# Performance work log

Measured on AMD Instinct MI355X. Metric: run time of the kernel, lower is better.

The kernel has to match this reference:

```python
import jax, jax.numpy as jnp
import numpy as np

N_NODES = 50000
N_EDGES = 640000
D_IN = 128
D_HID = 128
D_OUT = 128


def setup_inputs() -> dict:
    key = jax.random.key(0)
    k1, k2, k3, k4 = jax.random.split(key, 4)
    x = jax.random.normal(k1, (N_NODES, D_IN), dtype=jnp.float32)
    edge_index = jax.random.randint(k2, (2, N_EDGES), 0, N_NODES, dtype=jnp.int32)
    W1 = jax.random.normal(k3, (D_IN, D_HID), dtype=jnp.float32) * (1.0 / np.sqrt(D_IN))
    b1 = jnp.zeros((D_HID,), dtype=jnp.float32)
    W2 = jax.random.normal(k4, (D_HID, D_OUT), dtype=jnp.float32) * (1.0 / np.sqrt(D_HID))
    b2 = jnp.zeros((D_OUT,), dtype=jnp.float32)
    return {"x": x, "edge_index": edge_index, "W1": W1, "b1": b1, "W2": W2, "b2": b2}


def gcn_conv(x, edge_index, W, b, num_nodes):
    # PyG GCNConv: add self-loops, symmetric normalization, linear, aggregate, bias.
    loops = jnp.arange(num_nodes, dtype=edge_index.dtype)
    src = jnp.concatenate([edge_index[0], loops])  # source j
    dst = jnp.concatenate([edge_index[1], loops])  # target i
    deg = jax.ops.segment_sum(jnp.ones_like(dst, dtype=x.dtype), dst,
                              num_segments=num_nodes)  # in-degree incl. self-loop
    dinv = jnp.where(deg > 0, jax.lax.rsqrt(deg), 0.0)
    norm = dinv[src] * dinv[dst]  # [E+N]
    h = x @ W  # [N, hidden]
    msg = norm[:, None] * h[src]  # gather + scale
    out = jax.ops.segment_sum(msg, dst, num_segments=num_nodes)  # scatter-add
    return out + b


def reference(x, edge_index, W1, b1, W2, b2):
    h = gcn_conv(x, edge_index, W1, b1, x.shape[0])
    h = jnp.tanh(h)
    return h @ W2 + b2
```

## Files before the change

kernel.cpp:

```cpp
#include <hip/hip_runtime.h>


#define DFEAT 128
#define CAP 48
#define BROWS 32

typedef __attribute__((ext_vector_type(8))) short short8;
typedef __attribute__((ext_vector_type(4))) float float4v;

__device__ __forceinline__ float bflo(unsigned int u) {
    union { unsigned int i; float f; } v; v.i = u << 16; return v.f;
}
__device__ __forceinline__ float bfhi(unsigned int u) {
    union { unsigned int i; float f; } v; v.i = u & 0xffff0000u; return v.f;
}
__device__ __forceinline__ unsigned short f2bf(float f) {
    union { unsigned int i; float f; } v; v.f = f;
    unsigned int r = v.i + 0x7fffu + ((v.i >> 16) & 1u);
    return (unsigned short)(r >> 16);
}
__device__ __forceinline__ unsigned int pack2(float a, float b) {
    return (unsigned int)f2bf(a) | ((unsigned int)f2bf(b) << 16);
}
__device__ __forceinline__ float fast_tanh(float x) {
    float e = __expf(2.0f * x);
    float r = __builtin_amdgcn_rcpf(e + 1.0f);
    return __builtin_fmaf(-2.0f, r, 1.0f);
}

__global__ void k_count_scatter(const int* __restrict__ src, const int* __restrict__ dst,
                                int* __restrict__ cnt, int* __restrict__ col,
                                const float* __restrict__ W1, const float* __restrict__ W2,
                                unsigned short* __restrict__ w1f, unsigned short* __restrict__ w2f,
                                int e) {
    int i = blockIdx.x * blockDim.x + threadIdx.x;
    if (i < 2 * DFEAT * DFEAT) {
        int which = i >> 14;
        int idx = i & 16383;
        int k = idx >> 7, nn = idx & 127;
        int f = ((nn >> 4) << 2) + (k >> 5);
        int lane = (nn & 15) | (((k >> 3) & 3) << 4);
        int j = k & 7;
        int o = f * 512 + lane * 8 + j;
        if (which == 0) w1f[o] = f2bf(W1[idx]);
        else            w2f[o] = f2bf(W2[idx]);
    }
    if (i >= e) return;
    int d = dst[i];
    int p = atomicAdd(&cnt[d], 1);
    if (p < CAP) col[d * CAP + p] = src[i];
}

__global__ void k_prep(const float* __restrict__ x, const int* __restrict__ cnt,
                       unsigned int* __restrict__ xb2, int* __restrict__ col, int n) {
    int i = blockIdx.x * blockDim.x + threadIdx.x;
    if (i < n * 32) {
        float di = rsqrtf((float)(cnt[i >> 5] + 1));
        float4 v = ((const float4*)x)[i];
        xb2[i * 2]     = pack2(v.x * di, v.y * di);
        xb2[i * 2 + 1] = pack2(v.z * di, v.w * di);
    } else if (i < (n + 1) * 32) {
        xb2[i * 2] = 0u;
        xb2[i * 2 + 1] = 0u;
    }
    if (i < n) {
        int d = min(cnt[i], CAP);
        int dpad = (d + 3) & ~3;
        for (int p = d; p < dpad; ++p) col[i * CAP + p] = n;
    }
}

__global__ __launch_bounds__(256) void k_agg_gemm(
    const uint4* __restrict__ xb4, const int* __restrict__ cnt,
    const int* __restrict__ col,
    const unsigned short* __restrict__ w1f, const float* __restrict__ b1,
    const unsigned short* __restrict__ w2f, const float* __restrict__ b2,
    float* __restrict__ out, int n) {
    __shared__ unsigned short aggs[BROWS * 136];
    __shared__ unsigned short hs[BROWS * 136];
    const int t = threadIdx.x;

    const int lane16 = t & 15;
    const int sub = t >> 4;
    for (int g = 0; g < BROWS / 16; ++g) {
        int node_local = g * 16 + sub;
        int node = blockIdx.x * BROWS + node_local;
        int nodec = min(node, n - 1);
        uint4 v = xb4[(size_t)nodec * 16 + lane16];
        float a0 = bflo(v.x), a1 = bfhi(v.x), a2 = bflo(v.y), a3 = bfhi(v.y);
        float a4 = bflo(v.z), a5 = bfhi(v.z), a6 = bflo(v.w), a7 = bfhi(v.w);
        int deg = min(cnt[nodec], CAP);
        const int4* col4 = (const int4*)(col + (size_t)nodec * CAP);
        int nq = (deg + 3) >> 2;
        for (int q = 0; q < nq; ++q) {
            int4 s4 = col4[q];
            uint4 u0 = xb4[(size_t)s4.x * 16 + lane16];
            uint4 u1 = xb4[(size_t)s4.y * 16 + lane16];
            uint4 u2 = xb4[(size_t)s4.z * 16 + lane16];
            uint4 u3 = xb4[(size_t)s4.w * 16 + lane16];
            a0 += bflo(u0.x); a1 += bfhi(u0.x); a2 += bflo(u0.y); a3 += bfhi(u0.y);
            a4 += bflo(u0.z); a5 += bfhi(u0.z); a6 += bflo(u0.w); a7 += bfhi(u0.w);
            a0 += bflo(u1.x); a1 += bfhi(u1.x); a2 += bflo(u1.y); a3 += bfhi(u1.y);
            a4 += bflo(u1.z); a5 += bfhi(u1.z); a6 += bflo(u1.w); a7 += bfhi(u1.w);
            a0 += bflo(u2.x); a1 += bfhi(u2.x); a2 += bflo(u2.y); a3 += bfhi(u2.y);
            a4 += bflo(u2.z); a5 += bfhi(u2.z); a6 += bflo(u2.w); a7 += bfhi(u2.w);
            a0 += bflo(u3.x); a1 += bfhi(u3.x); a2 += bflo(u3.y); a3 += bfhi(u3.y);
            a4 += bflo(u3.z); a5 += bfhi(u3.z); a6 += bflo(u3.w); a7 += bfhi(u3.w);
        }
        float di = rsqrtf((float)(deg + 1));
        uint4 o;
        o.x = pack2(a0 * di, a1 * di);
        o.y = pack2(a2 * di, a3 * di);
        o.z = pack2(a4 * di, a5 * di);
        o.w = pack2(a6 * di, a7 * di);
        *(uint4*)&aggs[node_local * 136 + lane16 * 8] = o;
    }
    __syncthreads();

    const int wave = t >> 6, l = t & 63;
    const int strip = wave >> 1;
    const int colh = wave & 1;
    const int kq = l >> 4;
    const int lc = l & 15;
    const int row_local = strip * 16 + lc;

    float4v acc[4];
    for (int ct = 0; ct < 4; ++ct) acc[ct] = (float4v){0.f, 0.f, 0.f, 0.f};
    for (int kc = 0; kc < 4; ++kc) {
        short8 a = *(const short8*)(aggs + row_local * 136 + kc * 32 + kq * 8);
        for (int ct = 0; ct < 4; ++ct) {
            int ctg = colh * 4 + ct;
            short8 b = *(const short8*)(w1f + (ctg * 4 + kc) * 512 + l * 8);
            acc[ct] = __builtin_amdgcn_mfma_f32_16x16x32_bf16(a, b, acc[ct], 0, 0, 0);
        }
    }
    const int drow0 = strip * 16 + kq * 4;
    for (int ct = 0; ct < 4; ++ct) {
        int c = colh * 64 + ct * 16 + lc;
        float bb = b1[c];
        for (int r = 0; r < 4; ++r) {
            float v = fast_tanh(acc[ct][r] + bb);
            hs[(drow0 + r) * 136 + c] = f2bf(v);
        }
    }
    __syncthreads();

    float4v acc2[4];
    for (int ct = 0; ct < 4; ++ct) acc2[ct] = (float4v){0.f, 0.f, 0.f, 0.f};
    for (int kc = 0; kc < 4; ++kc) {
        short8 a = *(const short8*)(hs + row_local * 136 + kc * 32 + kq * 8);
        for (int ct = 0; ct < 4; ++ct) {
            int ctg = colh * 4 + ct;
            short8 b = *(const short8*)(w2f + (ctg * 4 + kc) * 512 + l * 8);
            acc2[ct] = __builtin_amdgcn_mfma_f32_16x16x32_bf16(a, b, acc2[ct], 0, 0, 0);
        }
    }
    const int orow0 = blockIdx.x * BROWS + drow0;
    for (int ct = 0; ct < 4; ++ct) {
        int c = colh * 64 + ct * 16 + lc;
        float bb = b2[c];
        for (int r = 0; r < 4; ++r) {
            int orow = orow0 + r;
            if (orow < n) out[(size_t)orow * DFEAT + c] = acc2[ct][r] + bb;
        }
    }
}

static inline size_t align256(size_t v) { return (v + 255) & ~(size_t)255; }

extern "C" void kernel_launch(void* const* d_in, const int* in_sizes, int n_in,
                              void* d_out, int out_size, void* d_ws, size_t ws_size,
                              hipStream_t stream) {
    const float* x  = (const float*)d_in[0];
    const int*   ei = (const int*)d_in[1];
    const float* W1 = (const float*)d_in[2];
    const float* b1 = (const float*)d_in[3];
    const float* W2 = (const float*)d_in[4];
    const float* b2 = (const float*)d_in[5];
    float* out = (float*)d_out;

    const int N = in_sizes[0] / DFEAT;
    const int E = in_sizes[1] / 2;
    const int* src = ei;
    const int* dst = ei + E;

    char* ws = (char*)d_ws;
    size_t off = 0;
    int* cnt = (int*)(ws + off);  off += align256((size_t)N * 4);
    int* col = (int*)(ws + off);  off += align256((size_t)N * CAP * 4);
    unsigned short* xb  = (unsigned short*)(ws + off); off += align256((size_t)(N + 1) * DFEAT * 2);
    unsigned short* w1f = (unsigned short*)(ws + off); off += align256((size_t)DFEAT * DFEAT * 2);
    unsigned short* w2f = (unsigned short*)(ws + off); off += align256((size_t)DFEAT * DFEAT * 2);

    hipMemsetAsync(cnt, 0, (size_t)N * 4, stream);
    k_count_scatter<<<(E + 255) / 256, 256, 0, stream>>>(
        src, dst, cnt, col, W1, W2, w1f, w2f, E);
    k_prep<<<((N + 1) * 32 + 255) / 256, 256, 0, stream>>>(
        x, cnt, (unsigned int*)xb, col, N);
    k_agg_gemm<<<(N + BROWS - 1) / BROWS, 256, 0, stream>>>(
        (const uint4*)xb, cnt, col, w1f, b1, w2f, b2, out, N);
}
```

Before: 161.7 us.

## Merge prep into scatter kernel and apply source degree scaling during aggregation

Merges the bf16 conversion of x into the edge-scatter kernel, which removes the separate prep launch, the zero pad row and the padding of column lists. The per-source normalisation dinv[src] is now computed inside the gather loop from cnt, using predicated duplicate indices with zero weight for tail slots. The column index load is software-prefetched one iteration ahead. The trade-off is an extra random cnt load per edge in the aggregation loop, in exchange for one fewer kernel launch and no dependency on the finished degree count before conversion.

```diff
diff --git a/kernel.cpp b/kernel.cpp
--- a/kernel.cpp
+++ b/kernel.cpp
@@ -28,11 +28,12 @@
     return __builtin_fmaf(-2.0f, r, 1.0f);
 }
 
-__global__ void k_count_scatter(const int* __restrict__ src, const int* __restrict__ dst,
-                                int* __restrict__ cnt, int* __restrict__ col,
-                                const float* __restrict__ W1, const float* __restrict__ W2,
-                                unsigned short* __restrict__ w1f, unsigned short* __restrict__ w2f,
-                                int e) {
+__global__ void k_scatter_conv(const int* __restrict__ src, const int* __restrict__ dst,
+                               int* __restrict__ cnt, int* __restrict__ col,
+                               const float* __restrict__ x, unsigned int* __restrict__ xb2,
+                               const float* __restrict__ W1, const float* __restrict__ W2,
+                               unsigned short* __restrict__ w1f, unsigned short* __restrict__ w2f,
+                               int e, int n32) {
     int i = blockIdx.x * blockDim.x + threadIdx.x;
     if (i < 2 * DFEAT * DFEAT) {
         int which = i >> 14;
@@ -45,28 +46,15 @@
         if (which == 0) w1f[o] = f2bf(W1[idx]);
         else            w2f[o] = f2bf(W2[idx]);
     }
-    if (i >= e) return;
-    int d = dst[i];
-    int p = atomicAdd(&cnt[d], 1);
-    if (p < CAP) col[d * CAP + p] = src[i];
-}
-
-__global__ void k_prep(const float* __restrict__ x, const int* __restrict__ cnt,
-                       unsigned int* __restrict__ xb2, int* __restrict__ col, int n) {
-    int i = blockIdx.x * blockDim.x + threadIdx.x;
-    if (i < n * 32) {
-        float di = rsqrtf((float)(cnt[i >> 5] + 1));
+    if (i < e) {
+        int d = dst[i];
+        int p = atomicAdd(&cnt[d], 1);
+        if (p < CAP) col[d * CAP + p] = src[i];
+    }
+    if (i < n32) {
         float4 v = ((const float4*)x)[i];
-        xb2[i * 2]     = pack2(v.x * di, v.y * di);
-        xb2[i * 2 + 1] = pack2(v.z * di, v.w * di);
-    } else if (i < (n + 1) * 32) {
-        xb2[i * 2] = 0u;
-        xb2[i * 2 + 1] = 0u;
-    }
-    if (i < n) {
-        int d = min(cnt[i], CAP);
-        int dpad = (d + 3) & ~3;
-        for (int p = d; p < dpad; ++p) col[i * CAP + p] = n;
+        xb2[i * 2]     = pack2(v.x, v.y);
+        xb2[i * 2 + 1] = pack2(v.z, v.w);
     }
 }
 
@@ -86,28 +74,51 @@
         int node_local = g * 16 + sub;
         int node = blockIdx.x * BROWS + node_local;
         int nodec = min(node, n - 1);
+        int raw = cnt[nodec];
+        int deg = min(raw, CAP);
+        float di = rsqrtf((float)(raw + 1));
         uint4 v = xb4[(size_t)nodec * 16 + lane16];
-        float a0 = bflo(v.x), a1 = bfhi(v.x), a2 = bflo(v.y), a3 = bfhi(v.y);
-        float a4 = bflo(v.z), a5 = bfhi(v.z), a6 = bflo(v.w), a7 = bfhi(v.w);
-        int deg = min(cnt[nodec], CAP);
+        float a0 = bflo(v.x) * di, a1 = bfhi(v.x) * di;
+        float a2 = bflo(v.y) * di, a3 = bfhi(v.y) * di;
+        float a4 = bflo(v.z) * di, a5 = bfhi(v.z) * di;
+        float a6 = bflo(v.w) * di, a7 = bfhi(v.w) * di;
         const int4* col4 = (const int4*)(col + (size_t)nodec * CAP);
         int nq = (deg + 3) >> 2;
+        int4 s4 = col4[0];
         for (int q = 0; q < nq; ++q) {
-            int4 s4 = col4[q];
-            uint4 u0 = xb4[(size_t)s4.x * 16 + lane16];
-            uint4 u1 = xb4[(size_t)s4.y * 16 + lane16];
-            uint4 u2 = xb4[(size_t)s4.z * 16 + lane16];
-            uint4 u3 = xb4[(size_t)s4.w * 16 + lane16];
-            a0 += bflo(u0.x); a1 += bfhi(u0.x); a2 += bflo(u0.y); a3 += bfhi(u0.y);
-            a4 += bflo(u0.z); a5 += bfhi(u0.z); a6 += bflo(u0.w); a7 += bfhi(u0.w);
-            a0 += bflo(u1.x); a1 += bfhi(u1.x); a2 += bflo(u1.y); a3 += bfhi(u1.y);
-            a4 += bflo(u1.z); a5 += bfhi(u1.z); a6 += bflo(u1.w); a7 += bfhi(u1.w);
-            a0 += bflo(u2.x); a1 += bfhi(u2.x); a2 += bflo(u2.y); a3 += bfhi(u2.y);
-            a4 += bflo(u2.z); a5 += bfhi(u2.z); a6 += bflo(u2.w); a7 += bfhi(u2.w);
-            a0 += bflo(u3.x); a1 += bfhi(u3.x); a2 += bflo(u3.y); a3 += bfhi(u3.y);
-            a4 += bflo(u3.z); a5 += bfhi(u3.z); a6 += bflo(u3.w); a7 += bfhi(u3.w);
-        }
-        float di = rsqrtf((float)(deg + 1));
+            int4 nx = col4[min(q + 1, nq - 1)];
+            int b4i = q * 4;
+            bool c1 = (b4i + 1) < deg, c2 = (b4i + 2) < deg, c3 = (b4i + 3) < deg;
+            int i0 = s4.x;
+            int i1 = c1 ? s4.y : i0;
+            int i2 = c2 ? s4.z : i0;
+            int i3 = c3 ? s4.w : i0;
+            float d0 = rsqrtf((float)(cnt[i0] + 1));
+            float d1 = c1 ? rsqrtf((float)(cnt[i1] + 1)) : 0.f;
+            float d2 = c2 ? rsqrtf((float)(cnt[i2] + 1)) : 0.f;
+            float d3 = c3 ? rsqrtf((float)(cnt[i3] + 1)) : 0.f;
+            uint4 u0 = xb4[(size_t)i0 * 16 + lane16];
+            uint4 u1 = xb4[(size_t)i1 * 16 + lane16];
+            uint4 u2 = xb4[(size_t)i2 * 16 + lane16];
+            uint4 u3 = xb4[(size_t)i3 * 16 + lane16];
+            a0 = __builtin_fmaf(bflo(u0.x), d0, a0); a1 = __builtin_fmaf(bfhi(u0.x), d0, a1);
+            a2 = __builtin_fmaf(bflo(u0.y), d0, a2); a3 = __builtin_fmaf(bfhi(u0.y), d0, a3);
+            a4 = __builtin_fmaf(bflo(u0.z), d0, a4); a5 = __builtin_fmaf(bfhi(u0.z), d0, a5);
+            a6 = __builtin_fmaf(bflo(u0.w), d0, a6); a7 = __builtin_fmaf(bfhi(u0.w), d0, a7);
+            a0 = __builtin_fmaf(bflo(u1.x), d1, a0); a1 = __builtin_fmaf(bfhi(u1.x), d1, a1);
+            a2 = __builtin_fmaf(bflo(u1.y), d1, a2); a3 = __builtin_fmaf(bfhi(u1.y), d1, a3);
+            a4 = __builtin_fmaf(bflo(u1.z), d1, a4); a5 = __builtin_fmaf(bfhi(u1.z), d1, a5);
+            a6 = __builtin_fmaf(bflo(u1.w), d1, a6); a7 = __builtin_fmaf(bfhi(u1.w), d1, a7);
+            a0 = __builtin_fmaf(bflo(u2.x), d2, a0); a1 = __builtin_fmaf(bfhi(u2.x), d2, a1);
+            a2 = __builtin_fmaf(bflo(u2.y), d2, a2); a3 = __builtin_fmaf(bfhi(u2.y), d2, a3);
+            a4 = __builtin_fmaf(bflo(u2.z), d2, a4); a5 = __builtin_fmaf(bfhi(u2.z), d2, a5);
+            a6 = __builtin_fmaf(bflo(u2.w), d2, a6); a7 = __builtin_fmaf(bfhi(u2.w), d2, a7);
+            a0 = __builtin_fmaf(bflo(u3.x), d3, a0); a1 = __builtin_fmaf(bfhi(u3.x), d3, a1);
+            a2 = __builtin_fmaf(bflo(u3.y), d3, a2); a3 = __builtin_fmaf(bfhi(u3.y), d3, a3);
+            a4 = __builtin_fmaf(bflo(u3.z), d3, a4); a5 = __builtin_fmaf(bfhi(u3.z), d3, a5);
+            a6 = __builtin_fmaf(bflo(u3.w), d3, a6); a7 = __builtin_fmaf(bfhi(u3.w), d3, a7);
+            s4 = nx;
+        }
         uint4 o;
         o.x = pack2(a0 * di, a1 * di);
         o.y = pack2(a2 * di, a3 * di);
@@ -188,15 +199,17 @@
     size_t off = 0;
     int* cnt = (int*)(ws + off);  off += align256((size_t)N * 4);
     int* col = (int*)(ws + off);  off += align256((size_t)N * CAP * 4);
-    unsigned short* xb  = (unsigned short*)(ws + off); off += align256((size_t)(N + 1) * DFEAT * 2);
+    unsigned short* xb  = (unsigned short*)(ws + off); off += align256((size_t)N * DFEAT * 2);
     unsigned short* w1f = (unsigned short*)(ws + off); off += align256((size_t)DFEAT * DFEAT * 2);
     unsigned short* w2f = (unsigned short*)(ws + off); off += align256((size_t)DFEAT * DFEAT * 2);
 
+    const int n32 = N * 32;
+    int total = n32 > E ? n32 : E;
+    if (total < 2 * DFEAT * DFEAT) total = 2 * DFEAT * DFEAT;
+
     hipMemsetAsync(cnt, 0, (size_t)N * 4, stream);
-    k_count_scatter<<<(E + 255) / 256, 256, 0, stream>>>(
-        src, dst, cnt, col, W1, W2, w1f, w2f, E);
-    k_prep<<<((N + 1) * 32 + 255) / 256, 256, 0, stream>>>(
-        x, cnt, (unsigned int*)xb, col, N);
+    k_scatter_conv<<<(total + 255) / 256, 256, 0, stream>>>(
+        src, dst, cnt, col, x, (unsigned int*)xb, W1, W2, w1f, w2f, E, n32);
     k_agg_gemm<<<(N + BROWS - 1) / BROWS, 256, 0, stream>>>(
         (const uint4*)xb, cnt, col, w1f, b1, w2f, b2, out, N);
 }
```

After: 165.1 us. +2.1%, slower.

## Split CSR build into count and scatter passes; unroll neighbor gather by eight

Applied to the files above, without the earlier changes.

The first kernel now pre-fills the whole neighbor table with the sentinel node index, zeroes a second counter array, and counts in-degrees. The second kernel converts x to scaled bf16 while scattering source indices with a separate atomic counter. Because every unused slot already holds the sentinel, the aggregation loop can fetch two int4 index groups and issue eight independent row gathers per iteration, keeping more loads in flight. The normalization now uses the uncapped degree. The cost is an extra pass of atomics over the edges, a full write of the index table, and some wasted gathers of the zero sentinel row when degrees are padded up to a multiple of eight.

```diff
diff --git a/kernel.cpp b/kernel.cpp
--- a/kernel.cpp
+++ b/kernel.cpp
@@ -28,11 +28,11 @@
     return __builtin_fmaf(-2.0f, r, 1.0f);
 }
 
-__global__ void k_count_scatter(const int* __restrict__ src, const int* __restrict__ dst,
-                                int* __restrict__ cnt, int* __restrict__ col,
-                                const float* __restrict__ W1, const float* __restrict__ W2,
-                                unsigned short* __restrict__ w1f, unsigned short* __restrict__ w2f,
-                                int e) {
+__global__ void k1_count_fill(const int* __restrict__ dst, int* __restrict__ cnt,
+                              int* __restrict__ cnt2, int4* __restrict__ col4,
+                              const float* __restrict__ W1, const float* __restrict__ W2,
+                              unsigned short* __restrict__ w1f, unsigned short* __restrict__ w2f,
+                              int e, int n, int ncol4) {
     int i = blockIdx.x * blockDim.x + threadIdx.x;
     if (i < 2 * DFEAT * DFEAT) {
         int which = i >> 14;
@@ -45,28 +45,33 @@
         if (which == 0) w1f[o] = f2bf(W1[idx]);
         else            w2f[o] = f2bf(W2[idx]);
     }
-    if (i >= e) return;
-    int d = dst[i];
-    int p = atomicAdd(&cnt[d], 1);
-    if (p < CAP) col[d * CAP + p] = src[i];
-}
-
-__global__ void k_prep(const float* __restrict__ x, const int* __restrict__ cnt,
-                       unsigned int* __restrict__ xb2, int* __restrict__ col, int n) {
+    if (i < ncol4) {
+        int4 s; s.x = n; s.y = n; s.z = n; s.w = n;
+        col4[i] = s;
+    }
+    if (i < (n + 3) / 4) ((int4*)cnt2)[i] = (int4){0, 0, 0, 0};
+    if (i < e) atomicAdd(&cnt[dst[i]], 1);
+}
+
+__global__ void k2_scatter_xb(const int* __restrict__ src, const int* __restrict__ dst,
+                              const int* __restrict__ cnt, int* __restrict__ cnt2,
+                              int* __restrict__ col,
+                              const float* __restrict__ x, unsigned int* __restrict__ xb2,
+                              int e, int n32) {
     int i = blockIdx.x * blockDim.x + threadIdx.x;
-    if (i < n * 32) {
+    if (i < n32) {
         float di = rsqrtf((float)(cnt[i >> 5] + 1));
         float4 v = ((const float4*)x)[i];
         xb2[i * 2]     = pack2(v.x * di, v.y * di);
         xb2[i * 2 + 1] = pack2(v.z * di, v.w * di);
-    } else if (i < (n + 1) * 32) {
+    } else if (i < n32 + 32) {
         xb2[i * 2] = 0u;
         xb2[i * 2 + 1] = 0u;
     }
-    if (i < n) {
-        int d = min(cnt[i], CAP);
-        int dpad = (d + 3) & ~3;
-        for (int p = d; p < dpad; ++p) col[i * CAP + p] = n;
+    if (i < e) {
+        int d = dst[i];
+        int p = atomicAdd(&cnt2[d], 1);
+        if (p < CAP) col[d * CAP + p] = src[i];
     }
 }
 
@@ -86,18 +91,25 @@
         int node_local = g * 16 + sub;
         int node = blockIdx.x * BROWS + node_local;
         int nodec = min(node, n - 1);
+        int raw = cnt[nodec];
+        int deg = min(raw, CAP);
+        float di = rsqrtf((float)(raw + 1));
         uint4 v = xb4[(size_t)nodec * 16 + lane16];
         float a0 = bflo(v.x), a1 = bfhi(v.x), a2 = bflo(v.y), a3 = bfhi(v.y);
         float a4 = bflo(v.z), a5 = bfhi(v.z), a6 = bflo(v.w), a7 = bfhi(v.w);
-        int deg = min(cnt[nodec], CAP);
         const int4* col4 = (const int4*)(col + (size_t)nodec * CAP);
-        int nq = (deg + 3) >> 2;
-        for (int q = 0; q < nq; ++q) {
-            int4 s4 = col4[q];
-            uint4 u0 = xb4[(size_t)s4.x * 16 + lane16];
-            uint4 u1 = xb4[(size_t)s4.y * 16 + lane16];
-            uint4 u2 = xb4[(size_t)s4.z * 16 + lane16];
-            uint4 u3 = xb4[(size_t)s4.w * 16 + lane16];
+        int nq2 = (deg + 7) >> 3;
+        for (int q = 0; q < nq2; ++q) {
+            int4 sa = col4[2 * q];
+            int4 sb = col4[2 * q + 1];
+            uint4 u0 = xb4[(size_t)sa.x * 16 + lane16];
+            uint4 u1 = xb4[(size_t)sa.y * 16 + lane16];
+            uint4 u2 = xb4[(size_t)sa.z * 16 + lane16];
+            uint4 u3 = xb4[(size_t)sa.w * 16 + lane16];
+            uint4 u4 = xb4[(size_t)sb.x * 16 + lane16];
+            uint4 u5 = xb4[(size_t)sb.y * 16 + lane16];
+            uint4 u6 = xb4[(size_t)sb.z * 16 + lane16];
+            uint4 u7 = xb4[(size_t)sb.w * 16 + lane16];
             a0 += bflo(u0.x); a1 += bfhi(u0.x); a2 += bflo(u0.y); a3 += bfhi(u0.y);
             a4 += bflo(u0.z); a5 += bfhi(u0.z); a6 += bflo(u0.w); a7 += bfhi(u0.w);
             a0 += bflo(u1.x); a1 += bfhi(u1.x); a2 += bflo(u1.y); a3 += bfhi(u1.y);
@@ -106,8 +118,15 @@
             a4 += bflo(u2.z); a5 += bfhi(u2.z); a6 += bflo(u2.w); a7 += bfhi(u2.w);
             a0 += bflo(u3.x); a1 += bfhi(u3.x); a2 += bflo(u3.y); a3 += bfhi(u3.y);
             a4 += bflo(u3.z); a5 += bfhi(u3.z); a6 += bflo(u3.w); a7 += bfhi(u3.w);
-        }
-        float di = rsqrtf((float)(deg + 1));
+            a0 += bflo(u4.x); a1 += bfhi(u4.x); a2 += bflo(u4.y); a3 += bfhi(u4.y);
+            a4 += bflo(u4.z); a5 += bfhi(u4.z); a6 += bflo(u4.w); a7 += bfhi(u4.w);
+            a0 += bflo(u5.x); a1 += bfhi(u5.x); a2 += bflo(u5.y); a3 += bfhi(u5.y);
+            a4 += bflo(u5.z); a5 += bfhi(u5.z); a6 += bflo(u5.w); a7 += bfhi(u5.w);
+            a0 += bflo(u6.x); a1 += bfhi(u6.x); a2 += bflo(u6.y); a3 += bfhi(u6.y);
+            a4 += bflo(u6.z); a5 += bfhi(u6.z); a6 += bflo(u6.w); a7 += bfhi(u6.w);
+            a0 += bflo(u7.x); a1 += bfhi(u7.x); a2 += bflo(u7.y); a3 += bfhi(u7.y);
+            a4 += bflo(u7.z); a5 += bfhi(u7.z); a6 += bflo(u7.w); a7 += bfhi(u7.w);
+        }
         uint4 o;
         o.x = pack2(a0 * di, a1 * di);
         o.y = pack2(a2 * di, a3 * di);
@@ -186,17 +205,25 @@
 
     char* ws = (char*)d_ws;
     size_t off = 0;
-    int* cnt = (int*)(ws + off);  off += align256((size_t)N * 4);
-    int* col = (int*)(ws + off);  off += align256((size_t)N * CAP * 4);
+    int* cnt  = (int*)(ws + off); off += align256((size_t)N * 4);
+    int* cnt2 = (int*)(ws + off); off += align256((size_t)N * 4);
+    int* col  = (int*)(ws + off); off += align256((size_t)N * CAP * 4);
     unsigned short* xb  = (unsigned short*)(ws + off); off += align256((size_t)(N + 1) * DFEAT * 2);
     unsigned short* w1f = (unsigned short*)(ws + off); off += align256((size_t)DFEAT * DFEAT * 2);
     unsigned short* w2f = (unsigned short*)(ws + off); off += align256((size_t)DFEAT * DFEAT * 2);
 
+    const int ncol4 = N * CAP / 4;
+    const int n32 = N * 32;
+
+    int t1 = E > ncol4 ? E : ncol4;
+    if (t1 < 2 * DFEAT * DFEAT) t1 = 2 * DFEAT * DFEAT;
+    int t2 = (n32 + 32) > E ? (n32 + 32) : E;
+
     hipMemsetAsync(cnt, 0, (size_t)N * 4, stream);
-    k_count_scatter<<<(E + 255) / 256, 256, 0, stream>>>(
-        src, dst, cnt, col, W1, W2, w1f, w2f, E);
-    k_prep<<<((N + 1) * 32 + 255) / 256, 256, 0, stream>>>(
-        x, cnt, (unsigned int*)xb, col, N);
+    k1_count_fill<<<(t1 + 255) / 256, 256, 0, stream>>>(
+        dst, cnt, cnt2, (int4*)col, W1, W2, w1f, w2f, E, N, ncol4);
+    k2_scatter_xb<<<(t2 + 255) / 256, 256, 0, stream>>>(
+        src, dst, cnt, cnt2, col, x, (unsigned int*)xb, E, n32);
     k_agg_gemm<<<(N + BROWS - 1) / BROWS, 256, 0, stream>>>(
         (const uint4*)xb, cnt, col, w1f, b1, w2f, b2, out, N);
 }
```

After: 195.0 us. +20.6%, slower.

## Pad degree counters to separate cache lines and gather eight neighbors per iteration

Applied to the files above, without the earlier changes.

Each node's atomic degree counter is moved to a 64-byte stride so that concurrent atomics on neighbouring nodes no longer contend on the same cache line. The aggregation loop now issues eight neighbour row loads per iteration instead of four, for more memory-level parallelism, and the column lists are padded to multiples of eight with the zero row. The counter buffer and its memset grow sixteenfold, and padding to eight adds wasted gathers for low-degree nodes. The launch size of the first kernel is also made to always cover the weight conversion.

```diff
diff --git a/kernel.cpp b/kernel.cpp
--- a/kernel.cpp
+++ b/kernel.cpp
@@ -3,6 +3,7 @@
 
 #define DFEAT 128
 #define CAP 48
+#define CSTR 16
 #define BROWS 32
 
 typedef __attribute__((ext_vector_type(8))) short short8;
@@ -47,7 +48,7 @@
     }
     if (i >= e) return;
     int d = dst[i];
-    int p = atomicAdd(&cnt[d], 1);
+    int p = atomicAdd(&cnt[d * CSTR], 1);
     if (p < CAP) col[d * CAP + p] = src[i];
 }
 
@@ -55,7 +56,7 @@
                        unsigned int* __restrict__ xb2, int* __restrict__ col, int n) {
     int i = blockIdx.x * blockDim.x + threadIdx.x;
     if (i < n * 32) {
-        float di = rsqrtf((float)(cnt[i >> 5] + 1));
+        float di = rsqrtf((float)(cnt[(i >> 5) * CSTR] + 1));
         float4 v = ((const float4*)x)[i];
         xb2[i * 2]     = pack2(v.x * di, v.y * di);
         xb2[i * 2 + 1] = pack2(v.z * di, v.w * di);
@@ -64,8 +65,8 @@
         xb2[i * 2 + 1] = 0u;
     }
     if (i < n) {
-        int d = min(cnt[i], CAP);
-        int dpad = (d + 3) & ~3;
+        int d = min(cnt[i * CSTR], CAP);
+        int dpad = (d + 7) & ~7;
         for (int p = d; p < dpad; ++p) col[i * CAP + p] = n;
     }
 }
@@ -86,18 +87,25 @@
         int node_local = g * 16 + sub;
         int node = blockIdx.x * BROWS + node_local;
         int nodec = min(node, n - 1);
+        int raw = cnt[nodec * CSTR];
+        int deg = min(raw, CAP);
+        float di = rsqrtf((float)(raw + 1));
         uint4 v = xb4[(size_t)nodec * 16 + lane16];
         float a0 = bflo(v.x), a1 = bfhi(v.x), a2 = bflo(v.y), a3 = bfhi(v.y);
         float a4 = bflo(v.z), a5 = bfhi(v.z), a6 = bflo(v.w), a7 = bfhi(v.w);
-        int deg = min(cnt[nodec], CAP);
         const int4* col4 = (const int4*)(col + (size_t)nodec * CAP);
-        int nq = (deg + 3) >> 2;
-        for (int q = 0; q < nq; ++q) {
-            int4 s4 = col4[q];
-            uint4 u0 = xb4[(size_t)s4.x * 16 + lane16];
-            uint4 u1 = xb4[(size_t)s4.y * 16 + lane16];
-            uint4 u2 = xb4[(size_t)s4.z * 16 + lane16];
-            uint4 u3 = xb4[(size_t)s4.w * 16 + lane16];
+        int nq2 = (deg + 7) >> 3;
+        for (int q = 0; q < nq2; ++q) {
+            int4 sa = col4[2 * q];
+            int4 sb = col4[2 * q + 1];
+            uint4 u0 = xb4[(size_t)sa.x * 16 + lane16];
+            uint4 u1 = xb4[(size_t)sa.y * 16 + lane16];
+            uint4 u2 = xb4[(size_t)sa.z * 16 + lane16];
+            uint4 u3 = xb4[(size_t)sa.w * 16 + lane16];
+            uint4 u4 = xb4[(size_t)sb.x * 16 + lane16];
+            uint4 u5 = xb4[(size_t)sb.y * 16 + lane16];
+            uint4 u6 = xb4[(size_t)sb.z * 16 + lane16];
+            uint4 u7 = xb4[(size_t)sb.w * 16 + lane16];
             a0 += bflo(u0.x); a1 += bfhi(u0.x); a2 += bflo(u0.y); a3 += bfhi(u0.y);
             a4 += bflo(u0.z); a5 += bfhi(u0.z); a6 += bflo(u0.w); a7 += bfhi(u0.w);
             a0 += bflo(u1.x); a1 += bfhi(u1.x); a2 += bflo(u1.y); a3 += bfhi(u1.y);
@@ -106,8 +114,15 @@
             a4 += bflo(u2.z); a5 += bfhi(u2.z); a6 += bflo(u2.w); a7 += bfhi(u2.w);
             a0 += bflo(u3.x); a1 += bfhi(u3.x); a2 += bflo(u3.y); a3 += bfhi(u3.y);
             a4 += bflo(u3.z); a5 += bfhi(u3.z); a6 += bflo(u3.w); a7 += bfhi(u3.w);
-        }
-        float di = rsqrtf((float)(deg + 1));
+            a0 += bflo(u4.x); a1 += bfhi(u4.x); a2 += bflo(u4.y); a3 += bfhi(u4.y);
+            a4 += bflo(u4.z); a5 += bfhi(u4.z); a6 += bflo(u4.w); a7 += bfhi(u4.w);
+            a0 += bflo(u5.x); a1 += bfhi(u5.x); a2 += bflo(u5.y); a3 += bfhi(u5.y);
+            a4 += bflo(u5.z); a5 += bfhi(u5.z); a6 += bflo(u5.w); a7 += bfhi(u5.w);
+            a0 += bflo(u6.x); a1 += bfhi(u6.x); a2 += bflo(u6.y); a3 += bfhi(u6.y);
+            a4 += bflo(u6.z); a5 += bfhi(u6.z); a6 += bflo(u6.w); a7 += bfhi(u6.w);
+            a0 += bflo(u7.x); a1 += bfhi(u7.x); a2 += bflo(u7.y); a3 += bfhi(u7.y);
+            a4 += bflo(u7.z); a5 += bfhi(u7.z); a6 += bflo(u7.w); a7 += bfhi(u7.w);
+        }
         uint4 o;
         o.x = pack2(a0 * di, a1 * di);
         o.y = pack2(a2 * di, a3 * di);
@@ -186,14 +201,16 @@
 
     char* ws = (char*)d_ws;
     size_t off = 0;
-    int* cnt = (int*)(ws + off);  off += align256((size_t)N * 4);
+    int* cnt = (int*)(ws + off);  off += align256((size_t)N * CSTR * 4);
     int* col = (int*)(ws + off);  off += align256((size_t)N * CAP * 4);
     unsigned short* xb  = (unsigned short*)(ws + off); off += align256((size_t)(N + 1) * DFEAT * 2);
     unsigned short* w1f = (unsigned short*)(ws + off); off += align256((size_t)DFEAT * DFEAT * 2);
     unsigned short* w2f = (unsigned short*)(ws + off); off += align256((size_t)DFEAT * DFEAT * 2);
 
-    hipMemsetAsync(cnt, 0, (size_t)N * 4, stream);
-    k_count_scatter<<<(E + 255) / 256, 256, 0, stream>>>(
+    int t1 = E > 2 * DFEAT * DFEAT ? E : 2 * DFEAT * DFEAT;
+
+    hipMemsetAsync(cnt, 0, (size_t)N * CSTR * 4, stream);
+    k_count_scatter<<<(t1 + 255) / 256, 256, 0, stream>>>(
         src, dst, cnt, col, W1, W2, w1f, w2f, E);
     k_prep<<<((N + 1) * 32 + 255) / 256, 256, 0, stream>>>(
         x, cnt, (unsigned int*)xb, col, N);
```

New measurement: 162.3 us. Within noise of the previous version (+0.4%).
